# Kernel optimization log

Measured on AMD Instinct MI355X. Metric: run time of the kernel, lower is better.

## Reference

```python
import jax, jax.numpy as jnp
import numpy as np

R = 5.0      # cutoff radius (init arg)
N = 4096     # total atoms
B = 8        # number of periodic systems in the batch


def setup_inputs() -> dict:
    key = jax.random.key(0)
    k1, k2, k3 = jax.random.split(key, 3)
    # positions in a ~20 Angstrom box (matches cell scale)
    pos = jax.random.uniform(k1, (N, 3), dtype=jnp.float32) * 20.0
    # sorted per-atom graph ids, as produced by a batched molecular loader
    batch = jnp.sort(jax.random.randint(k2, (N,), 0, B))
    # near-cubic 20A cells with small triclinic perturbation (well-conditioned)
    cell = jnp.eye(3, dtype=jnp.float32) * 20.0 + 0.5 * jax.random.normal(k3, (B, 3, 3), dtype=jnp.float32)
    return {"pos": pos, "cell": cell, "batch": batch}


def reference(pos, cell, batch):
    # Dense, fixed-shape equivalent of RadiusGraph.forward with PBC cell wrap.
    # Original returns dynamically filtered (edge_index, disp); here we return
    # the full [N,N,3] displacement grid (masked to 0 off-graph) plus the
    # boolean edge mask -- same math, jit-compatible static shapes.
    n = pos.shape[0]
    disp = pos[:, None, :] - pos[None, :, :]            # [N,N,3], row i minus col j
    # PBC minimum-image wrap: per edge, cell is taken from the ROW node's graph
    cell_n = cell[batch]                                # [N,3,3]
    inv_cellT = jnp.linalg.inv(jnp.swapaxes(cell_n, 1, 2))   # [N,3,3] = (cell^T)^{-1}
    # scaled = solve(cell^T, disp) vectorized over all pairs
    scaled = jnp.einsum('iab,ijb->ija', inv_cellT, disp)     # [N,N,3]
    disp = disp - jnp.einsum('iab,ijb->ija', cell_n, jnp.round(scaled))
    # edge validity: same graph, no self-loop, within cutoff (after wrap)
    same_graph = batch[:, None] == batch[None, :]
    not_self = ~jnp.eye(n, dtype=bool)
    mask = same_graph & not_self & (jnp.linalg.norm(disp, axis=-1) < R)
    disp = jnp.where(mask[..., None], disp, jnp.zeros((), disp.dtype))
    return disp, mask
```

## Files before the change

### kernel.cpp

```cpp
#include <hip/hip_runtime.h>
#include <math.h>

#define NATOMS 4096
#define R_CUT 5.0f
#define JPT 4
#define BLOCK 256
#define JPB (BLOCK * JPT)
#define IPB 8

__global__ __launch_bounds__(BLOCK) void radius_graph_kernel(
    const float* __restrict__ pos,
    const float* __restrict__ cell,
    const int*   __restrict__ batch,
    float* __restrict__ disp_out,
    float* __restrict__ mask_out)
{
    __shared__ float sBuf[2 * JPB * 3];

    const int bid = blockIdx.x;
    const int rg  = bid >> 2;
    const int jc  = bid & 3;
    const int tid = (int)threadIdx.x;

    const int j0 = jc * JPB + tid * JPT;

    const float4* pj = (const float4*)(pos + (size_t)j0 * 3);
    const float4 q0 = pj[0], q1 = pj[1], q2 = pj[2];
    const int4 bj4 = *(const int4*)(batch + j0);

    const float pjx[4] = { q0.x, q0.w, q1.z, q2.y };
    const float pjy[4] = { q0.y, q1.x, q1.w, q2.z };
    const float pjz[4] = { q0.z, q1.y, q2.x, q2.w };
    const int   bj[4]  = { bj4.x, bj4.y, bj4.z, bj4.w };

    const int i0 = rg * IPB;

    #pragma unroll 1
    for (int r = 0; r < IPB; ++r) {
        const int i = i0 + r;

        const int bi = batch[i];
        const float pix = pos[i * 3 + 0];
        const float piy = pos[i * 3 + 1];
        const float piz = pos[i * 3 + 2];

        const float* C = cell + (size_t)bi * 9;
        const float C00 = C[0], C01 = C[1], C02 = C[2];
        const float C10 = C[3], C11 = C[4], C12 = C[5];
        const float C20 = C[6], C21 = C[7], C22 = C[8];
        const float cof00 =  (C11 * C22 - C12 * C21);
        const float cof01 = -(C10 * C22 - C12 * C20);
        const float cof02 =  (C10 * C21 - C11 * C20);
        const float cof10 = -(C01 * C22 - C02 * C21);
        const float cof11 =  (C00 * C22 - C02 * C20);
        const float cof12 = -(C00 * C21 - C01 * C20);
        const float cof20 =  (C01 * C12 - C02 * C11);
        const float cof21 = -(C00 * C12 - C02 * C10);
        const float cof22 =  (C00 * C11 - C01 * C10);
        const float det = C00 * cof00 + C01 * cof01 + C02 * cof02;
        const float id  = 1.0f / det;
        const float A00 = cof00 * id, A01 = cof01 * id, A02 = cof02 * id;
        const float A10 = cof10 * id, A11 = cof11 * id, A12 = cof12 * id;
        const float A20 = cof20 * id, A21 = cof21 * id, A22 = cof22 * id;

        float od[12];
        float om[4];

        #pragma unroll
        for (int t = 0; t < 4; ++t) {
            const int j = j0 + t;
            const float d0 = __fsub_rn(pix, pjx[t]);
            const float d1 = __fsub_rn(piy, pjy[t]);
            const float d2 = __fsub_rn(piz, pjz[t]);

            const float s0 = __fadd_rn(__fadd_rn(__fmul_rn(A00, d0), __fmul_rn(A01, d1)), __fmul_rn(A02, d2));
            const float s1 = __fadd_rn(__fadd_rn(__fmul_rn(A10, d0), __fmul_rn(A11, d1)), __fmul_rn(A12, d2));
            const float s2 = __fadd_rn(__fadd_rn(__fmul_rn(A20, d0), __fmul_rn(A21, d1)), __fmul_rn(A22, d2));

            const float r0 = rintf(s0);
            const float r1 = rintf(s1);
            const float r2 = rintf(s2);

            const float w0 = __fsub_rn(d0, __fadd_rn(__fadd_rn(__fmul_rn(C00, r0), __fmul_rn(C01, r1)), __fmul_rn(C02, r2)));
            const float w1 = __fsub_rn(d1, __fadd_rn(__fadd_rn(__fmul_rn(C10, r0), __fmul_rn(C11, r1)), __fmul_rn(C12, r2)));
            const float w2 = __fsub_rn(d2, __fadd_rn(__fadd_rn(__fmul_rn(C20, r0), __fmul_rn(C21, r1)), __fmul_rn(C22, r2)));

            const float n2 = __fadd_rn(__fadd_rn(__fmul_rn(w0, w0), __fmul_rn(w1, w1)), __fmul_rn(w2, w2));
            const bool m = (bi == bj[t]) && (i != j) && (sqrtf(n2) < R_CUT);

            od[t * 3 + 0] = m ? w0 : 0.0f;
            od[t * 3 + 1] = m ? w1 : 0.0f;
            od[t * 3 + 2] = m ? w2 : 0.0f;
            om[t] = m ? 1.0f : 0.0f;
        }

        float4* lb = (float4*)sBuf + (size_t)(r & 1) * (JPB * 3 / 4);
        lb[tid * 3 + 0] = make_float4(od[0], od[1], od[2],  od[3]);
        lb[tid * 3 + 1] = make_float4(od[4], od[5], od[6],  od[7]);
        lb[tid * 3 + 2] = make_float4(od[8], od[9], od[10], od[11]);

        float4* mout = (float4*)(mask_out + (size_t)i * NATOMS + (size_t)jc * JPB);
        mout[tid] = make_float4(om[0], om[1], om[2], om[3]);

        asm volatile("s_waitcnt lgkmcnt(0)\n\ts_barrier" ::: "memory");

        float4* gb = (float4*)(disp_out + (size_t)i * (NATOMS * 3) + (size_t)jc * (JPB * 3));
        gb[0 * BLOCK + tid] = lb[0 * BLOCK + tid];
        gb[1 * BLOCK + tid] = lb[1 * BLOCK + tid];
        gb[2 * BLOCK + tid] = lb[2 * BLOCK + tid];
    }
}

extern "C" void kernel_launch(void* const* d_in, const int* in_sizes, int n_in,
                              void* d_out, int out_size, void* d_ws, size_t ws_size,
                              hipStream_t stream) {
    const float* pos   = (const float*)d_in[0];
    const float* cell  = (const float*)d_in[1];
    const int*   batch = (const int*)d_in[2];

    float* disp_out = (float*)d_out;
    float* mask_out = (float*)d_out + (size_t)NATOMS * NATOMS * 3;

    const int blocks = (NATOMS / IPB) * (NATOMS / JPB);
    radius_graph_kernel<<<blocks, BLOCK, 0, stream>>>(pos, cell, batch, disp_out, mask_out);
}
```

Baseline: 261.4 us.

## Drop LDS staging and store displacements directly with strided 12-byte writes

Removes the shared-memory staging buffer and the per-row barrier, and remaps each thread's j elements from 4 contiguous atoms to 4 atoms strided by the block size. Displacements are now written straight to global memory as 3-float vectors and the mask as scalar floats, so each wave's writes are still contiguous across lanes. This cuts LDS traffic and synchronisation, but trades 16-byte vector stores for 12-byte and 4-byte stores, which may lower store efficiency in this write-bound kernel.

Result: no change. 261.7 us (+0.1%).

```diff
diff --git a/kernel.cpp b/kernel.cpp
--- a/kernel.cpp
+++ b/kernel.cpp
@@ -8,6 +8,8 @@
 #define JPB (BLOCK * JPT)
 #define IPB 8
 
+typedef float f3 __attribute__((ext_vector_type(3), aligned(4)));
+
 __global__ __launch_bounds__(BLOCK) void radius_graph_kernel(
     const float* __restrict__ pos,
     const float* __restrict__ cell,
@@ -15,23 +17,21 @@
     float* __restrict__ disp_out,
     float* __restrict__ mask_out)
 {
-    __shared__ float sBuf[2 * JPB * 3];
-
     const int bid = blockIdx.x;
     const int rg  = bid >> 2;
     const int jc  = bid & 3;
     const int tid = (int)threadIdx.x;
 
-    const int j0 = jc * JPB + tid * JPT;
-
-    const float4* pj = (const float4*)(pos + (size_t)j0 * 3);
-    const float4 q0 = pj[0], q1 = pj[1], q2 = pj[2];
-    const int4 bj4 = *(const int4*)(batch + j0);
-
-    const float pjx[4] = { q0.x, q0.w, q1.z, q2.y };
-    const float pjy[4] = { q0.y, q1.x, q1.w, q2.z };
-    const float pjz[4] = { q0.z, q1.y, q2.x, q2.w };
-    const int   bj[4]  = { bj4.x, bj4.y, bj4.z, bj4.w };
+    float pjx[JPT], pjy[JPT], pjz[JPT];
+    int   bj[JPT];
+    #pragma unroll
+    for (int k = 0; k < JPT; ++k) {
+        const int j = jc * JPB + k * BLOCK + tid;
+        pjx[k] = pos[j * 3 + 0];
+        pjy[k] = pos[j * 3 + 1];
+        pjz[k] = pos[j * 3 + 2];
+        bj[k]  = batch[j];
+    }
 
     const int i0 = rg * IPB;
 
@@ -63,15 +63,15 @@
         const float A10 = cof10 * id, A11 = cof11 * id, A12 = cof12 * id;
         const float A20 = cof20 * id, A21 = cof21 * id, A22 = cof22 * id;
 
-        float od[12];
-        float om[4];
+        const size_t rowm = (size_t)i * NATOMS;
+        const size_t rowd = rowm * 3;
 
         #pragma unroll
-        for (int t = 0; t < 4; ++t) {
-            const int j = j0 + t;
-            const float d0 = __fsub_rn(pix, pjx[t]);
-            const float d1 = __fsub_rn(piy, pjy[t]);
-            const float d2 = __fsub_rn(piz, pjz[t]);
+        for (int k = 0; k < JPT; ++k) {
+            const int j = jc * JPB + k * BLOCK + tid;
+            const float d0 = __fsub_rn(pix, pjx[k]);
+            const float d1 = __fsub_rn(piy, pjy[k]);
+            const float d2 = __fsub_rn(piz, pjz[k]);
 
             const float s0 = __fadd_rn(__fadd_rn(__fmul_rn(A00, d0), __fmul_rn(A01, d1)), __fmul_rn(A02, d2));
             const float s1 = __fadd_rn(__fadd_rn(__fmul_rn(A10, d0), __fmul_rn(A11, d1)), __fmul_rn(A12, d2));
@@ -86,28 +86,15 @@
             const float w2 = __fsub_rn(d2, __fadd_rn(__fadd_rn(__fmul_rn(C20, r0), __fmul_rn(C21, r1)), __fmul_rn(C22, r2)));
 
             const float n2 = __fadd_rn(__fadd_rn(__fmul_rn(w0, w0), __fmul_rn(w1, w1)), __fmul_rn(w2, w2));
-            const bool m = (bi == bj[t]) && (i != j) && (sqrtf(n2) < R_CUT);
+            const bool m = (bi == bj[k]) && (i != j) && (sqrtf(n2) < R_CUT);
 
-            od[t * 3 + 0] = m ? w0 : 0.0f;
-            od[t * 3 + 1] = m ? w1 : 0.0f;
-            od[t * 3 + 2] = m ? w2 : 0.0f;
-            om[t] = m ? 1.0f : 0.0f;
+            f3 v;
+            v.x = m ? w0 : 0.0f;
+            v.y = m ? w1 : 0.0f;
+            v.z = m ? w2 : 0.0f;
+            *(f3*)(disp_out + rowd + (size_t)j * 3) = v;
+            mask_out[rowm + (size_t)j] = m ? 1.0f : 0.0f;
         }
-
-        float4* lb = (float4*)sBuf + (size_t)(r & 1) * (JPB * 3 / 4);
-        lb[tid * 3 + 0] = make_float4(od[0], od[1], od[2],  od[3]);
-        lb[tid * 3 + 1] = make_float4(od[4], od[5], od[6],  od[7]);
-        lb[tid * 3 + 2] = make_float4(od[8], od[9], od[10], od[11]);
-
-        float4* mout = (float4*)(mask_out + (size_t)i * NATOMS + (size_t)jc * JPB);
-        mout[tid] = make_float4(om[0], om[1], om[2], om[3]);
-
-        asm volatile("s_waitcnt lgkmcnt(0)\n\ts_barrier" ::: "memory");
-
-        float4* gb = (float4*)(disp_out + (size_t)i * (NATOMS * 3) + (size_t)jc * (JPB * 3));
-        gb[0 * BLOCK + tid] = lb[0 * BLOCK + tid];
-        gb[1 * BLOCK + tid] = lb[1 * BLOCK + tid];
-        gb[2 * BLOCK + tid] = lb[2 * BLOCK + tid];
     }
 }
 
```
